# Performance work log

Measured on AMD Instinct MI355X. Metric: run time of the kernel, lower is better.

## Reference

```python
import jax, jax.numpy as jnp
import numpy as np

EPS = 1e-6
H, KV, HD, FF = 16, 8, 128, 3072

def rmsnorm(x, scale):
    # qwen3_compatible: compute in fp32, scale, cast back
    xf = x.astype(jnp.float32)
    var = jnp.mean(xf * xf, axis=-1, keepdims=True)
    return ((xf * jax.lax.rsqrt(var + EPS)) * scale).astype(x.dtype)

def apply_rope(x, cos, sin):
    # x: [b, h, s, d]; cos/sin: [s, d]
    d = x.shape[-1]
    x1, x2 = x[..., : d // 2], x[..., d // 2 :]
    rotated = jnp.concatenate([-x2, x1], axis=-1)
    return (x * cos[None, None] + rotated * sin[None, None]).astype(x.dtype)

def setup_inputs() -> dict:
    key = jax.random.key(0)
    B, S, D = 2, 2048, 1024
    ks = jax.random.split(key, 8)
    x = jax.random.normal(ks[0], (B, S, D), jnp.float32)
    mask = jnp.triu(jnp.ones((S, S), dtype=bool), k=1)  # True = masked (causal)
    # Qwen3 RoPE, base 1e6, full-dim cos/sin (halves duplicated)
    pos = jnp.arange(S, dtype=jnp.float32)
    inv_freq = 1.0 / (1e6 ** (jnp.arange(0, HD, 2, dtype=jnp.float32) / HD))
    ang = pos[:, None] * inv_freq[None, :]
    cos = jnp.concatenate([jnp.cos(ang), jnp.cos(ang)], axis=-1)
    sin = jnp.concatenate([jnp.sin(ang), jnp.sin(ang)], axis=-1)
    s = 0.02
    wq = jax.random.normal(ks[1], (D, H * HD), jnp.float32) * s
    wk = jax.random.normal(ks[2], (D, KV * HD), jnp.float32) * s
    wv = jax.random.normal(ks[3], (D, KV * HD), jnp.float32) * s
    wo = jax.random.normal(ks[4], (H * HD, D), jnp.float32) * s
    fc1 = jax.random.normal(ks[5], (D, FF), jnp.float32) * s
    fc2 = jax.random.normal(ks[6], (D, FF), jnp.float32) * s
    fc3 = jax.random.normal(ks[7], (FF, D), jnp.float32) * s
    return dict(x=x, mask=mask, cos=cos, sin=sin, wq=wq, wk=wk, wv=wv, wo=wo,
                fc1=fc1, fc2=fc2, fc3=fc3,
                norm1_scale=jnp.ones((D,), jnp.float32),
                norm2_scale=jnp.ones((D,), jnp.float32),
                q_norm_scale=jnp.ones((HD,), jnp.float32),
                k_norm_scale=jnp.ones((HD,), jnp.float32))

def reference(x, mask, cos, sin, wq, wk, wv, wo, fc1, fc2, fc3,
              norm1_scale, norm2_scale, q_norm_scale, k_norm_scale):
    B, S, D = x.shape
    G = H // KV  # GQA group size
    # --- attention sublayer ---
    h = rmsnorm(x, norm1_scale)
    q = (h @ wq).reshape(B, S, H, HD).transpose(0, 2, 1, 3)   # [b,h,s,d]
    k = (h @ wk).reshape(B, S, KV, HD).transpose(0, 2, 1, 3)  # [b,kv,s,d]
    v = (h @ wv).reshape(B, S, KV, HD).transpose(0, 2, 1, 3)
    q = rmsnorm(q, q_norm_scale)
    k = rmsnorm(k, k_norm_scale)
    q = apply_rope(q, cos, sin)
    k = apply_rope(k, cos, sin)
    k = jnp.repeat(k, G, axis=1)  # repeat_interleave over head dim
    v = jnp.repeat(v, G, axis=1)
    scores = jnp.einsum('bhqd,bhkd->bhqk', q, k)
    scores = jnp.where(mask[None, None], -jnp.inf, scores)
    w = jax.nn.softmax(scores / np.float32(np.sqrt(HD)), axis=-1)
    ctx = jnp.einsum('bhqk,bhkd->bqhd', w, v).reshape(B, S, H * HD)
    x = x + ctx @ wo
    # --- SwiGLU FFN sublayer ---
    h2 = rmsnorm(x, norm2_scale)
    ff = (jax.nn.silu(h2 @ fc1) * (h2 @ fc2)) @ fc3
    return x + ff
```

## Files before the change

### kernel.cpp

```cpp
#include <hip/hip_runtime.h>

#define B_  2
#define S_  2048
#define D_  1024
#define H_  16
#define KV_ 8
#define HD_ 128
#define FF_ 3072
#define KVB 32

typedef short bf16x8 __attribute__((ext_vector_type(8)));
typedef short bf16x4 __attribute__((ext_vector_type(4)));
typedef float f32x4 __attribute__((ext_vector_type(4)));

__device__ __forceinline__ float bf2f(unsigned short u) {
    union { float f; unsigned int i; } c; c.i = ((unsigned int)u) << 16; return c.f;
}
__device__ __forceinline__ unsigned short f2bf(float f) {
    union { float f; unsigned int i; } c; c.f = f;
    unsigned int r = c.i + 0x7fffu + ((c.i >> 16) & 1u);
    return (unsigned short)(r >> 16);
}

__device__ __forceinline__ void gload_lds16(const unsigned short* g, char* ldsbase) {
    __builtin_amdgcn_global_load_lds(
        (const __attribute__((address_space(1))) unsigned int*)g,
        (__attribute__((address_space(3))) unsigned int*)ldsbase, 16, 0, 0);
}

__device__ __forceinline__ f32x4 pv_mfma(bf16x4 a, bf16x4 b, f32x4 c) {
#if __has_builtin(__builtin_amdgcn_mfma_f32_16x16x16bf16_1k)
    return __builtin_amdgcn_mfma_f32_16x16x16bf16_1k(a, b, c, 0, 0, 0);
#elif __has_builtin(__builtin_amdgcn_mfma_f32_16x16x16_bf16)
    return __builtin_amdgcn_mfma_f32_16x16x16_bf16(a, b, c, 0, 0, 0);
#else
    f32x4 d;
    asm("v_mfma_f32_16x16x16_bf16 %0, %1, %2, %3" : "=v"(d) : "v"(a), "v"(b), "v"(c));
    return d;
#endif
}

__global__ __launch_bounds__(256)
void rmsnorm_kernel(const float* __restrict__ in, const float* __restrict__ scale,
                    unsigned short* __restrict__ out) {
    const int row = blockIdx.x;
    const int t = threadIdx.x;
    const float4 v = *reinterpret_cast<const float4*>(in + (size_t)row * D_ + t * 4);
    float s = v.x * v.x + v.y * v.y + v.z * v.z + v.w * v.w;
    #pragma unroll
    for (int o = 32; o; o >>= 1) s += __shfl_down(s, o);
    __shared__ float red[4];
    const int lane = t & 63, wid = t >> 6;
    if (lane == 0) red[wid] = s;
    __syncthreads();
    s = red[0] + red[1] + red[2] + red[3];
    const float rn = rsqrtf(s * (1.0f / D_) + 1e-6f);
    const float4 sc = *reinterpret_cast<const float4*>(scale + t * 4);
    unsigned short o4[4];
    o4[0] = f2bf(v.x * rn * sc.x);
    o4[1] = f2bf(v.y * rn * sc.y);
    o4[2] = f2bf(v.z * rn * sc.z);
    o4[3] = f2bf(v.w * rn * sc.w);
    *reinterpret_cast<ushort4*>(out + (size_t)row * D_ + t * 4) =
        *reinterpret_cast<ushort4*>(o4);
}

__global__ __launch_bounds__(256)
void wtrans_kernel(const float* __restrict__ W, unsigned short* __restrict__ Wt,
                   int K, int N) {
    __shared__ float tile[32][33];
    const int t = threadIdx.x;
    const int kt = blockIdx.x * 32, nt = blockIdx.y * 32;
    {
        const int r = t >> 3, c4 = (t & 7) * 4;
        const float4 v = *reinterpret_cast<const float4*>(W + (size_t)(kt + r) * N + nt + c4);
        tile[r][c4] = v.x; tile[r][c4 + 1] = v.y; tile[r][c4 + 2] = v.z; tile[r][c4 + 3] = v.w;
    }
    __syncthreads();
    {
        const int n = t >> 3, k4 = (t & 7) * 4;
        unsigned short o[4];
        #pragma unroll
        for (int i = 0; i < 4; i++) o[i] = f2bf(tile[k4 + i][n]);
        *reinterpret_cast<ushort4*>(Wt + (size_t)(nt + n) * K + kt + k4) =
            *reinterpret_cast<ushort4*>(o);
    }
}

__global__ __launch_bounds__(512, 2)
void gemm256(const unsigned short* __restrict__ A, const unsigned short* __restrict__ Bt,
             unsigned short* __restrict__ C, int M, int N, int K, int nm) {
    __shared__ __align__(16) char lds[131072];
    const int tid = threadIdx.x;
    const int lane = tid & 63, w = tid >> 6;
    const int lm = lane & 15, lg = lane >> 4;
    const int wr = w >> 2, wc = w & 3;
    const int nwg = gridDim.x;
    const int cpx = nwg >> 3;
    const int bid = blockIdx.x;
    const int swz = (bid & 7) * cpx + (bid >> 3);
    const int m0 = (swz % nm) * 256;
    const int n0 = (swz / nm) * 256;

    f32x4 acc[8][4];
    #pragma unroll
    for (int i = 0; i < 8; ++i)
        #pragma unroll
        for (int j = 0; j < 4; ++j) acc[i][j] = (f32x4){0.f, 0.f, 0.f, 0.f};

    const int srow = tid >> 3;
    const int skel = ((tid & 7) * 8) ^ (((tid >> 5) & 1) << 4);
    const int flip = ((lm >> 2) & 1) << 5;
    const int abase = (wr * 128 + lm) * 128 + ((lg * 16) ^ flip);
    const int bbase = (wc * 64 + lm) * 128 + ((lg * 16) ^ flip);

    auto stage = [&](int kt, int d) {
        const unsigned short* ga = A + (size_t)(m0 + srow) * K + kt * 64 + skel;
        const unsigned short* gb = Bt + (size_t)(n0 + srow) * K + kt * 64 + skel;
        char* la = lds + d * 65536 + (w << 10);
        char* lb = la + 32768;
        #pragma unroll
        for (int c = 0; c < 4; ++c) {
            gload_lds16(ga + (size_t)(c * 64) * K, la + c * 8192);
            gload_lds16(gb + (size_t)(c * 64) * K, lb + c * 8192);
        }
    };

    stage(0, 0);
    __syncthreads();

    const int ntile = K >> 6;
    for (int kt = 0; kt < ntile; ++kt) {
        const int d = kt & 1;
        if (kt + 1 < ntile) stage(kt + 1, d ^ 1);
        const char* Ar = lds + d * 65536;
        const char* Br = Ar + 32768;
        bf16x8 bb[4][2];
        #pragma unroll
        for (int nf = 0; nf < 4; ++nf)
            #pragma unroll
            for (int s = 0; s < 2; ++s)
                bb[nf][s] = *reinterpret_cast<const bf16x8*>(Br + bbase + nf * 2048 + s * 64);
        bf16x8 aH[4][2];
        #pragma unroll
        for (int f = 0; f < 4; ++f)
            #pragma unroll
            for (int s = 0; s < 2; ++s)
                aH[f][s] = *reinterpret_cast<const bf16x8*>(Ar + abase + f * 2048 + s * 64);
        #pragma unroll
        for (int f = 0; f < 4; ++f)
            #pragma unroll
            for (int nf = 0; nf < 4; ++nf)
                #pragma unroll
                for (int s = 0; s < 2; ++s)
                    acc[f][nf] = __builtin_amdgcn_mfma_f32_16x16x32_bf16(
                        aH[f][s], bb[nf][s], acc[f][nf], 0, 0, 0);
        #pragma unroll
        for (int f = 0; f < 4; ++f)
            #pragma unroll
            for (int s = 0; s < 2; ++s)
                aH[f][s] = *reinterpret_cast<const bf16x8*>(Ar + abase + 8192 + f * 2048 + s * 64);
        #pragma unroll
        for (int f = 0; f < 4; ++f)
            #pragma unroll
            for (int nf = 0; nf < 4; ++nf)
                #pragma unroll
                for (int s = 0; s < 2; ++s)
                    acc[4 + f][nf] = __builtin_amdgcn_mfma_f32_16x16x32_bf16(
                        aH[f][s], bb[nf][s], acc[4 + f][nf], 0, 0, 0);
        __syncthreads();
    }

    #pragma unroll
    for (int mf = 0; mf < 8; ++mf)
        #pragma unroll
        for (int nf = 0; nf < 4; ++nf)
            #pragma unroll
            for (int r = 0; r < 4; ++r)
                C[(size_t)(m0 + wr * 128 + mf * 16 + lg * 4 + r) * N +
                  (n0 + wc * 64 + nf * 16 + lm)] = f2bf(acc[mf][nf][r]);
}

template<int EPI>
__global__ __launch_bounds__(256)
void gemm_bt(const unsigned short* __restrict__ A, const unsigned short* __restrict__ Bt,
             void* __restrict__ Cout, const float* __restrict__ resid,
             int M, int N, int K, int lda) {
    constexpr int SMB = (EPI == 2) ? 34816 : 16384;
    __shared__ __align__(16) char sm[SMB];
    const int t = threadIdx.x;
    const int lane = t & 63, w = t >> 6;
    const int m0 = blockIdx.x * 128, n0 = blockIdx.y * 128;
    const int wr = w >> 1, wc = w & 1;
    const int lm = lane & 15, lg = lane >> 4;

    f32x4 acc[4][4];
    #pragma unroll
    for (int i = 0; i < 4; i++)
        #pragma unroll
        for (int j = 0; j < 4; j++) acc[i][j] = (f32x4){0.f, 0.f, 0.f, 0.f};

    const int row0 = t >> 2, kseg = (t & 3) * 8;
    const unsigned short* Ab = A + (size_t)(m0 + row0) * lda + kseg;
    const unsigned short* Bb = Bt + (size_t)(n0 + row0) * K + kseg;
    const size_t rstepA = (size_t)64 * lda;
    const size_t rstepB = (size_t)64 * K;
    char* ldsA = sm + w * 1024;
    char* ldsB = sm + 8192 + w * 1024;

    for (int k0 = 0; k0 < K; k0 += 32) {
        gload_lds16(Ab + k0, ldsA);
        gload_lds16(Ab + rstepA + k0, ldsA + 4096);
        gload_lds16(Bb + k0, ldsB);
        gload_lds16(Bb + rstepB + k0, ldsB + 4096);
        __syncthreads();
        bf16x8 aF[4], bF[4];
        #pragma unroll
        for (int i = 0; i < 4; i++)
            aF[i] = *reinterpret_cast<const bf16x8*>(sm + (wr * 64 + i * 16 + lm) * 64 + lg * 16);
        #pragma unroll
        for (int j = 0; j < 4; j++)
            bF[j] = *reinterpret_cast<const bf16x8*>(sm + 8192 + (wc * 64 + j * 16 + lm) * 64 + lg * 16);
        #pragma unroll
        for (int i = 0; i < 4; i++)
            #pragma unroll
            for (int j = 0; j < 4; j++)
                acc[i][j] = __builtin_amdgcn_mfma_f32_16x16x32_bf16(aF[i], bF[j], acc[i][j], 0, 0, 0);
        __syncthreads();
    }

    if (EPI == 2) {
        unsigned short (*Ct)[136] = reinterpret_cast<unsigned short(*)[136]>(sm);
        #pragma unroll
        for (int i = 0; i < 4; i++)
            #pragma unroll
            for (int j = 0; j < 4; j++)
                #pragma unroll
                for (int r = 0; r < 4; r++)
                    Ct[wc * 64 + j * 16 + lm][wr * 64 + i * 16 + lg * 4 + r] = f2bf(acc[i][j][r]);
        __syncthreads();
        const int colr = t >> 1, seg = t & 1;
        unsigned short* dst = reinterpret_cast<unsigned short*>(Cout) +
                              (size_t)(n0 + colr) * M + m0 + seg * 64;
        const unsigned short* srcp = &Ct[colr][seg * 64];
        #pragma unroll
        for (int i = 0; i < 8; i++)
            reinterpret_cast<uint4*>(dst)[i] = reinterpret_cast<const uint4*>(srcp)[i];
        return;
    }

    #pragma unroll
    for (int i = 0; i < 4; i++) {
        #pragma unroll
        for (int j = 0; j < 4; j++) {
            #pragma unroll
            for (int r = 0; r < 4; r++) {
                const int row = m0 + wr * 64 + i * 16 + lg * 4 + r;
                const int col = n0 + wc * 64 + j * 16 + lm;
                const size_t idx = (size_t)row * N + col;
                if (EPI == 0) {
                    reinterpret_cast<unsigned short*>(Cout)[idx] = f2bf(acc[i][j][r]);
                } else {
                    reinterpret_cast<float*>(Cout)[idx] = resid[idx] + acc[i][j][r];
                }
            }
        }
    }
}

__global__ __launch_bounds__(128)
void qknorm_rope_kernel(unsigned short* __restrict__ qk, const float* __restrict__ scale,
                        const float* __restrict__ cosb, const float* __restrict__ sinb,
                        int ld) {
    const int row = blockIdx.x;
    const int head = blockIdx.y;
    const int s = row & (S_ - 1);
    const int t = threadIdx.x;
    unsigned short* p = qk + (size_t)row * ld + head * HD_;
    const float v = bf2f(p[t]);
    float ss = v * v;
    #pragma unroll
    for (int o = 32; o; o >>= 1) ss += __shfl_down(ss, o);
    __shared__ float red[2];
    __shared__ float vals[HD_];
    const int lane = t & 63, wid = t >> 6;
    if (lane == 0) red[wid] = ss;
    __syncthreads();
    ss = red[0] + red[1];
    const float rn = rsqrtf(ss * (1.0f / HD_) + 1e-6f);
    const float nv = v * rn * scale[t];
    vals[t] = nv;
    __syncthreads();
    const float rot = (t < 64) ? -vals[t + 64] : vals[t - 64];
    const float c = cosb[(size_t)s * HD_ + t];
    const float sn = sinb[(size_t)s * HD_ + t];
    p[t] = f2bf(nv * c + rot * sn);
}

__global__ __launch_bounds__(256)
void fattn_kernel(const unsigned short* __restrict__ qg,
                  const unsigned short* __restrict__ kg,
                  const unsigned short* __restrict__ vtg,
                  unsigned short* __restrict__ out, int qld, int kld) {
    __shared__ __align__(16) char klds[2 * 8192];
    __shared__ __align__(16) char vtlds[2 * 9216];
    const int t = threadIdx.x;
    const int lane = t & 63, w = t >> 6;
    const int lm = lane & 15, lg = lane >> 4;
    const int g = blockIdx.x;
    const int h = g & 15, b = g >> 4;
    const int qt = (int)gridDim.y - 1 - (int)blockIdx.y;
    const int kvh = h >> 1;
    const int q0b = qt * 64;
    const int q0w = q0b + w * 16;
    const float CS = 0.12752409731504826f;

    const unsigned short* qbase = qg + (size_t)(b * S_ + q0w + lm) * qld + h * HD_;
    bf16x8 qf[4];
    #pragma unroll
    for (int kk = 0; kk < 4; ++kk)
        qf[kk] = *reinterpret_cast<const bf16x8*>(qbase + kk * 32 + lg * 8);

    f32x4 acc[8];
    #pragma unroll
    for (int i = 0; i < 8; ++i) acc[i] = (f32x4){0.f, 0.f, 0.f, 0.f};
    float m = -3e38f, l = 0.f;

    const int nt = 2 * qt + 2;
    const int skv = t >> 3, sd8 = t & 7;
    const int vd = t >> 1, vseg = t & 1;
    const unsigned short* kgb = kg + (size_t)b * S_ * kld + kvh * HD_;
    const unsigned short* vgb = vtg + (size_t)(kvh * HD_) * (B_ * S_) + (size_t)b * S_;

    uint4 kr0, kr1, vr0, vr1;
    auto LOADR = [&](int kt) {
        const int kv0 = kt * KVB;
        const unsigned short* ksrc = kgb + (size_t)(kv0 + skv) * kld + sd8 * 16;
        kr0 = *reinterpret_cast<const uint4*>(ksrc);
        kr1 = *reinterpret_cast<const uint4*>(ksrc + 8);
        const unsigned short* vsrc = vgb + (size_t)vd * (B_ * S_) + kv0 + vseg * 16;
        vr0 = *reinterpret_cast<const uint4*>(vsrc);
        vr1 = *reinterpret_cast<const uint4*>(vsrc + 8);
    };
    auto WRITELDS = [&](int bufi) {
        char* kd = klds + bufi * 8192 + skv * 256;
        const int sw = (skv & 7) << 4;
        *reinterpret_cast<uint4*>(kd + ((sd8 * 32) ^ sw)) = kr0;
        *reinterpret_cast<uint4*>(kd + ((sd8 * 32 + 16) ^ sw)) = kr1;
        char* vdst = vtlds + bufi * 9216 + vd * 72 + vseg * 32;
        *reinterpret_cast<uint2*>(vdst)      = make_uint2(vr0.x, vr0.y);
        *reinterpret_cast<uint2*>(vdst + 8)  = make_uint2(vr0.z, vr0.w);
        *reinterpret_cast<uint2*>(vdst + 16) = make_uint2(vr1.x, vr1.y);
        *reinterpret_cast<uint2*>(vdst + 24) = make_uint2(vr1.z, vr1.w);
    };

    LOADR(0);
    WRITELDS(0);
    __syncthreads();

    for (int kt = 0; kt < nt; ++kt) {
        const int kv0 = kt * KVB;
        const int bufi = kt & 1;
        const bool havenext = (kt + 1 < nt);
        if (havenext) LOADR(kt + 1);
        if (kv0 <= q0w + 15) {
            f32x4 st[2];
            st[0] = (f32x4){0.f, 0.f, 0.f, 0.f};
            st[1] = (f32x4){0.f, 0.f, 0.f, 0.f};
            #pragma unroll
            for (int sub = 0; sub < 2; ++sub) {
                const int kvl = sub * 16 + lm;
                const char* krow = klds + bufi * 8192 + kvl * 256;
                const int sw = (kvl & 7) << 4;
                #pragma unroll
                for (int kk = 0; kk < 4; ++kk) {
                    const bf16x8 kf = *reinterpret_cast<const bf16x8*>(krow + ((kk * 64 + lg * 16) ^ sw));
                    st[sub] = __builtin_amdgcn_mfma_f32_16x16x32_bf16(kf, qf[kk], st[sub], 0, 0, 0);
                }
            }
            if (kv0 + KVB - 1 > q0w) {
                const int qa = q0w + lm;
                #pragma unroll
                for (int sub = 0; sub < 2; ++sub)
                    #pragma unroll
                    for (int r = 0; r < 4; ++r)
                        if (kv0 + sub * 16 + lg * 4 + r > qa) st[sub][r] = -3e38f;
            }
            float pmax = st[0][0];
            #pragma unroll
            for (int r = 1; r < 4; ++r) pmax = fmaxf(pmax, st[0][r]);
            #pragma unroll
            for (int r = 0; r < 4; ++r) pmax = fmaxf(pmax, st[1][r]);
            pmax = fmaxf(pmax, __shfl_xor(pmax, 16));
            pmax = fmaxf(pmax, __shfl_xor(pmax, 32));
            if (__any(pmax - m > 8.0f)) {
                const float mn = fmaxf(pmax, m);
                const float corr = exp2f((m - mn) * CS);
                l *= corr;
                #pragma unroll
                for (int i = 0; i < 8; ++i) acc[i] *= corr;
                m = mn;
            }
            float ps = 0.f;
            bf16x4 pb[2];
            #pragma unroll
            for (int sub = 0; sub < 2; ++sub)
                #pragma unroll
                for (int r = 0; r < 4; ++r) {
                    const float pv = exp2f((st[sub][r] - m) * CS);
                    ps += pv;
                    pb[sub][r] = (short)f2bf(pv);
                }
            ps += __shfl_xor(ps, 16);
            ps += __shfl_xor(ps, 32);
            l += ps;
            #pragma unroll
            for (int sub = 0; sub < 2; ++sub) {
                const char* vb2 = vtlds + bufi * 9216 + sub * 32 + lg * 8;
                #pragma unroll
                for (int db = 0; db < 8; ++db) {
                    const bf16x4 vf = *reinterpret_cast<const bf16x4*>(vb2 + (db * 16 + lm) * 72);
                    acc[db] = pv_mfma(vf, pb[sub], acc[db]);
                }
            }
        }
        if (havenext) WRITELDS((kt + 1) & 1);
        __syncthreads();
    }
    const float inv = 1.0f / l;
    unsigned short* ob = out + (size_t)(b * S_ + q0w + lm) * qld + h * HD_ + lg * 4;
    #pragma unroll
    for (int db = 0; db < 8; ++db) {
        unsigned short r4[4];
        #pragma unroll
        for (int r = 0; r < 4; ++r) r4[r] = f2bf(acc[db][r] * inv);
        *reinterpret_cast<uint2*>(ob + db * 16) = *reinterpret_cast<uint2*>(r4);
    }
}

__global__ __launch_bounds__(256)
void silu_mul_kernel(unsigned short* __restrict__ g, int n4) {
    const int i = blockIdx.x * 256 + threadIdx.x;
    if (i >= n4) return;
    const int r = i / (FF_ / 4);
    const int c = (i - r * (FF_ / 4)) * 4;
    const size_t off = (size_t)r * (2 * FF_) + c;
    const uint2 a = *reinterpret_cast<const uint2*>(g + off);
    const uint2 bv = *reinterpret_cast<const uint2*>(g + off + FF_);
    const unsigned int au[2] = {a.x, a.y}, bu[2] = {bv.x, bv.y};
    unsigned int rr[2];
    #pragma unroll
    for (int j = 0; j < 2; j++) {
        const float a0 = bf2f((unsigned short)(au[j] & 0xffff));
        const float a1 = bf2f((unsigned short)(au[j] >> 16));
        const float b0 = bf2f((unsigned short)(bu[j] & 0xffff));
        const float b1 = bf2f((unsigned short)(bu[j] >> 16));
        const float s0 = a0 / (1.f + __expf(-a0)) * b0;
        const float s1 = a1 / (1.f + __expf(-a1)) * b1;
        rr[j] = ((unsigned int)f2bf(s1) << 16) | (unsigned int)f2bf(s0);
    }
    *reinterpret_cast<uint2*>(g + off) = make_uint2(rr[0], rr[1]);
}

extern "C" void kernel_launch(void* const* d_in, const int* in_sizes, int n_in,
                              void* d_out, int out_size, void* d_ws, size_t ws_size,
                              hipStream_t stream) {
    const float* x    = (const float*)d_in[0];
    const float* cosb = (const float*)d_in[2];
    const float* sinb = (const float*)d_in[3];
    const float* wq   = (const float*)d_in[4];
    const float* wk   = (const float*)d_in[5];
    const float* wv   = (const float*)d_in[6];
    const float* wo   = (const float*)d_in[7];
    const float* fc1  = (const float*)d_in[8];
    const float* fc2  = (const float*)d_in[9];
    const float* fc3  = (const float*)d_in[10];
    const float* n1s  = (const float*)d_in[11];
    const float* n2s  = (const float*)d_in[12];
    const float* qns  = (const float*)d_in[13];
    const float* kns  = (const float*)d_in[14];

    char* ws = (char*)d_ws;
    const int M = B_ * S_;
    float* outf = (float*)d_out;

    unsigned short* h    = (unsigned short*)(ws);
    unsigned short* qkb  = (unsigned short*)(ws + 8388608);
    unsigned short* vtb  = (unsigned short*)(ws + 33554432);
    unsigned short* g12  = (unsigned short*)(ws + 8388608);
    float*          x2   = (float*)(ws + 58720256);
    unsigned short* wqkt = (unsigned short*)(ws + 75497472);
    unsigned short* wvt  = (unsigned short*)(ws + 81788928);
    unsigned short* wot  = (unsigned short*)(ws + 83886080);
    unsigned short* f12t = (unsigned short*)(ws + 88080384);
    unsigned short* f3t  = (unsigned short*)(ws + 100663296);
    unsigned short* wqt = wqkt;
    unsigned short* wkt = wqkt + (size_t)2048 * 1024;
    unsigned short* f1t = f12t;
    unsigned short* f2t = f12t + (size_t)3072 * 1024;

    wtrans_kernel<<<dim3(D_ / 32, (H_ * HD_) / 32), 256, 0, stream>>>(wq, wqt, D_, H_ * HD_);
    wtrans_kernel<<<dim3(D_ / 32, (KV_ * HD_) / 32), 256, 0, stream>>>(wk, wkt, D_, KV_ * HD_);
    wtrans_kernel<<<dim3(D_ / 32, (KV_ * HD_) / 32), 256, 0, stream>>>(wv, wvt, D_, KV_ * HD_);
    wtrans_kernel<<<dim3((H_ * HD_) / 32, D_ / 32), 256, 0, stream>>>(wo, wot, H_ * HD_, D_);
    wtrans_kernel<<<dim3(D_ / 32, FF_ / 32), 256, 0, stream>>>(fc1, f1t, D_, FF_);
    wtrans_kernel<<<dim3(D_ / 32, FF_ / 32), 256, 0, stream>>>(fc2, f2t, D_, FF_);
    wtrans_kernel<<<dim3(FF_ / 32, D_ / 32), 256, 0, stream>>>(fc3, f3t, FF_, D_);

    rmsnorm_kernel<<<M, 256, 0, stream>>>(x, n1s, h);
    gemm256<<<(M / 256) * (3072 / 256), 512, 0, stream>>>(h, wqkt, qkb, M, 3072, D_, M / 256);
    gemm_bt<2><<<dim3(M / 128, (KV_ * HD_) / 128), 256, 0, stream>>>(h, wvt, vtb, nullptr, M, KV_ * HD_, D_, D_);
    qknorm_rope_kernel<<<dim3(M, H_), 128, 0, stream>>>(qkb, qns, cosb, sinb, 3072);
    qknorm_rope_kernel<<<dim3(M, KV_), 128, 0, stream>>>(qkb + 2048, kns, cosb, sinb, 3072);
    fattn_kernel<<<dim3(H_ * B_, S_ / 64), 256, 0, stream>>>(qkb, qkb + 2048, vtb, qkb, 3072, 3072);
    gemm_bt<1><<<dim3(M / 128, D_ / 128), 256, 0, stream>>>(qkb, wot, x2, x, M, D_, H_ * HD_, 3072);
    rmsnorm_kernel<<<M, 256, 0, stream>>>(x2, n2s, h);
    gemm256<<<(M / 256) * (6144 / 256), 512, 0, stream>>>(h, f12t, g12, M, 6144, D_, M / 256);
    silu_mul_kernel<<<(M * FF_ / 4 + 255) / 256, 256, 0, stream>>>(g12, M * FF_ / 4);
    gemm_bt<1><<<dim3(M / 128, D_ / 128), 256, 0, stream>>>(g12, f3t, outf, x2, M, D_, FF_, 2 * FF_);
}
```

Measured before the change: 423.9 us.

## Split GEMM prefetch into two phases interleaved with MFMA, with explicit vmcnt waits

```diff
diff --git a/kernel.cpp b/kernel.cpp
--- a/kernel.cpp
+++ b/kernel.cpp
@@ -114,25 +114,34 @@
     const int abase = (wr * 128 + lm) * 128 + ((lg * 16) ^ flip);
     const int bbase = (wc * 64 + lm) * 128 + ((lg * 16) ^ flip);
 
-    auto stage = [&](int kt, int d) {
+    auto part1 = [&](int kt, int d) {
         const unsigned short* ga = A + (size_t)(m0 + srow) * K + kt * 64 + skel;
         const unsigned short* gb = Bt + (size_t)(n0 + srow) * K + kt * 64 + skel;
         char* la = lds + d * 65536 + (w << 10);
         char* lb = la + 32768;
-        #pragma unroll
-        for (int c = 0; c < 4; ++c) {
-            gload_lds16(ga + (size_t)(c * 64) * K, la + c * 8192);
-            gload_lds16(gb + (size_t)(c * 64) * K, lb + c * 8192);
-        }
+        gload_lds16(gb,                      lb);
+        gload_lds16(gb + (size_t)64 * K,     lb + 8192);
+        gload_lds16(gb + (size_t)128 * K,    lb + 16384);
+        gload_lds16(gb + (size_t)192 * K,    lb + 24576);
+        gload_lds16(ga,                      la);
+        gload_lds16(ga + (size_t)128 * K,    la + 16384);
     };
-
-    stage(0, 0);
-    __syncthreads();
+    auto part2 = [&](int kt, int d) {
+        const unsigned short* ga = A + (size_t)(m0 + srow) * K + kt * 64 + skel;
+        char* la = lds + d * 65536 + (w << 10);
+        gload_lds16(ga + (size_t)64 * K,     la + 8192);
+        gload_lds16(ga + (size_t)192 * K,    la + 24576);
+    };
+
+    part1(0, 0);
+    part2(0, 0);
+    asm volatile("s_waitcnt vmcnt(0)" ::: "memory");
+    __builtin_amdgcn_s_barrier();
 
     const int ntile = K >> 6;
     for (int kt = 0; kt < ntile; ++kt) {
         const int d = kt & 1;
-        if (kt + 1 < ntile) stage(kt + 1, d ^ 1);
+        const bool pf = (kt + 1 < ntile);
         const char* Ar = lds + d * 65536;
         const char* Br = Ar + 32768;
         bf16x8 bb[4][2];
@@ -147,6 +156,8 @@
             #pragma unroll
             for (int s = 0; s < 2; ++s)
                 aH[f][s] = *reinterpret_cast<const bf16x8*>(Ar + abase + f * 2048 + s * 64);
+        if (pf) part1(kt + 1, d ^ 1);
+        __builtin_amdgcn_s_setprio(1);
         #pragma unroll
         for (int f = 0; f < 4; ++f)
             #pragma unroll
@@ -155,11 +166,17 @@
                 for (int s = 0; s < 2; ++s)
                     acc[f][nf] = __builtin_amdgcn_mfma_f32_16x16x32_bf16(
                         aH[f][s], bb[nf][s], acc[f][nf], 0, 0, 0);
+        __builtin_amdgcn_s_setprio(0);
+        if (pf) asm volatile("s_waitcnt vmcnt(6)" ::: "memory");
+        else    asm volatile("s_waitcnt vmcnt(0)" ::: "memory");
+        __builtin_amdgcn_s_barrier();
         #pragma unroll
         for (int f = 0; f < 4; ++f)
             #pragma unroll
             for (int s = 0; s < 2; ++s)
                 aH[f][s] = *reinterpret_cast<const bf16x8*>(Ar + abase + 8192 + f * 2048 + s * 64);
+        if (pf) part2(kt + 1, d ^ 1);
+        __builtin_amdgcn_s_setprio(1);
         #pragma unroll
         for (int f = 0; f < 4; ++f)
             #pragma unroll
@@ -168,7 +185,11 @@
                 for (int s = 0; s < 2; ++s)
                     acc[4 + f][nf] = __builtin_amdgcn_mfma_f32_16x16x32_bf16(
                         aH[f][s], bb[nf][s], acc[4 + f][nf], 0, 0, 0);
-        __syncthreads();
+        __builtin_amdgcn_s_setprio(0);
+        if (pf) {
+            asm volatile("s_waitcnt vmcnt(2)" ::: "memory");
+            __builtin_amdgcn_s_barrier();
+        }
     }
 
     #pragma unroll
```

New measurement: 422.3 us. About the same (-0.4%).
